# Kernel optimization log

Measured on AMD Instinct MI355X. Metric: run time of the kernel, lower is better.

The kernel has to match this reference:

```python
import jax, jax.numpy as jnp
import numpy as np

B, C, H, W = 4, 256, 64, 64

def setup_inputs() -> dict:
    key = jax.random.key(0)
    ks = jax.random.split(key, 6)
    inv = 1.0 / np.sqrt(C)
    return {
        "feature": jax.random.normal(ks[0], (B, C, H, W), dtype=jnp.float32),
        "flow": jax.random.normal(ks[1], (B, 2, H, W), dtype=jnp.float32),
        "q_w": jax.random.uniform(ks[2], (C, C), dtype=jnp.float32, minval=-inv, maxval=inv),
        "q_b": jax.random.uniform(ks[3], (C,), dtype=jnp.float32, minval=-inv, maxval=inv),
        "k_w": jax.random.uniform(ks[4], (C, C), dtype=jnp.float32, minval=-inv, maxval=inv),
        "k_b": jax.random.uniform(ks[5], (C,), dtype=jnp.float32, minval=-inv, maxval=inv),
    }

def reference(feature, flow, q_w, q_b, k_w, k_b):
    b, c, h, w = feature.shape
    # [b,c,h,w] -> [b, h*w, c] tokens
    tok = feature.reshape(b, c, h * w).transpose(0, 2, 1)
    v = flow.reshape(b, 2, h * w).transpose(0, 2, 1)       # [b, hw, 2]
    q = jnp.einsum('bnc,dc->bnd', tok, q_w) + q_b           # Linear(c,c)
    k = jnp.einsum('bnc,dc->bnd', tok, k_w) + k_b
    scale = 1.0 / jnp.sqrt(jnp.asarray(c, dtype=q.dtype))
    scores = jnp.einsum('bld,bsd->bls', q, k) * scale       # [b, hw, hw]
    attn = jax.nn.softmax(scores, axis=-1)                  # dropout_p=0 -> no-op
    out = jnp.einsum('bls,bsv->blv', attn, v)               # [b, hw, 2]
    return out.reshape(b, h, w, 2).transpose(0, 3, 1, 2)    # [b, 2, h, w]
```

## Files before the change

### kernel.cpp

```cpp
#include <hip/hip_runtime.h>
#include <math.h>

#define BB 4
#define CC 256
#define HWN 4096
#define NTOK 16384
#define SCQ 0.09016844136f

typedef __attribute__((ext_vector_type(8))) short short8;
typedef __attribute__((ext_vector_type(4))) float f32x4;
typedef unsigned short ushort_t;

__device__ __forceinline__ ushort_t f2bf(float f) {
    unsigned int u = __float_as_uint(f);
    unsigned int r = (u + 0x7FFFu + ((u >> 16) & 1u)) >> 16;
    return (ushort_t)r;
}
__device__ __forceinline__ unsigned int pack2(float a, float b) {
    return (unsigned int)f2bf(a) | ((unsigned int)f2bf(b) << 16);
}

__global__ __launch_bounds__(256, 2) void proj_kernel(
    const float* __restrict__ feature,
    const float* __restrict__ q_w, const float* __restrict__ k_w,
    const float* __restrict__ q_bias, const float* __restrict__ k_bias,
    ushort_t* __restrict__ qb, ushort_t* __restrict__ kb,
    float* __restrict__ zbuf)
{
    int gid = blockIdx.x * 256 + threadIdx.x;
    if (gid < 3 * NTOK) zbuf[gid] = 0.f;

    int tt = blockIdx.x & 63;
    int b  = blockIdx.x >> 6;
    int tok0 = tt * 64;

    int t = threadIdx.x, w = t >> 6, lane = t & 63;
    int n16 = lane & 15, quad = lane >> 4;

    __shared__ float    lsA[64][69];
    __shared__ ushort_t lsB[64][264];

    const float* F = feature + (size_t)(b * CC) * HWN;

    int cl = t >> 2, tg = (t & 3) * 16;
    int tokw = t >> 2, c16 = (t & 3) * 16;

    for (int ch = 0; ch < 4; ch++) {
        const float* src = F + (size_t)(ch * 64 + cl) * HWN + tok0 + tg;
        *(float4*)&lsA[cl][tg]      = *(const float4*)(src);
        *(float4*)&lsA[cl][tg + 4]  = *(const float4*)(src + 4);
        *(float4*)&lsA[cl][tg + 8]  = *(const float4*)(src + 8);
        *(float4*)&lsA[cl][tg + 12] = *(const float4*)(src + 12);
        __syncthreads();
        #pragma unroll
        for (int jj = 0; jj < 8; jj++)
            *(unsigned int*)&lsB[tokw][ch * 64 + c16 + 2 * jj] =
                pack2(lsA[c16 + 2 * jj][tokw], lsA[c16 + 2 * jj + 1][tokw]);
        __syncthreads();
    }

    int dw0 = w * 64;
    #pragma unroll
    for (int dsub = 0; dsub < 4; dsub++) {
        int d0 = dw0 + dsub * 16;
        f32x4 accq[4], acck[4];
        #pragma unroll
        for (int i = 0; i < 4; i++) {
            accq[i] = (f32x4){0.f, 0.f, 0.f, 0.f};
            acck[i] = (f32x4){0.f, 0.f, 0.f, 0.f};
        }
        #pragma unroll
        for (int kc = 0; kc < 8; kc++) {
            size_t off = (size_t)(d0 + n16) * CC + kc * 32 + quad * 8;
            float4 a0 = *(const float4*)&q_w[off];
            float4 a1 = *(const float4*)&q_w[off + 4];
            short8 aq, ak;
            aq[0] = (short)f2bf(a0.x * SCQ); aq[1] = (short)f2bf(a0.y * SCQ);
            aq[2] = (short)f2bf(a0.z * SCQ); aq[3] = (short)f2bf(a0.w * SCQ);
            aq[4] = (short)f2bf(a1.x * SCQ); aq[5] = (short)f2bf(a1.y * SCQ);
            aq[6] = (short)f2bf(a1.z * SCQ); aq[7] = (short)f2bf(a1.w * SCQ);
            a0 = *(const float4*)&k_w[off];
            a1 = *(const float4*)&k_w[off + 4];
            ak[0] = (short)f2bf(a0.x); ak[1] = (short)f2bf(a0.y);
            ak[2] = (short)f2bf(a0.z); ak[3] = (short)f2bf(a0.w);
            ak[4] = (short)f2bf(a1.x); ak[5] = (short)f2bf(a1.y);
            ak[6] = (short)f2bf(a1.z); ak[7] = (short)f2bf(a1.w);
            #pragma unroll
            for (int tokt = 0; tokt < 4; tokt++) {
                short8 bf = *(const short8*)&lsB[tokt * 16 + n16][kc * 32 + quad * 8];
                accq[tokt] = __builtin_amdgcn_mfma_f32_16x16x32_bf16(aq, bf, accq[tokt], 0, 0, 0);
                acck[tokt] = __builtin_amdgcn_mfma_f32_16x16x32_bf16(ak, bf, acck[tokt], 0, 0, 0);
            }
        }
        float bqv[4], bkv[4];
        #pragma unroll
        for (int r = 0; r < 4; r++) {
            bqv[r] = q_bias[d0 + quad * 4 + r] * SCQ;
            bkv[r] = k_bias[d0 + quad * 4 + r];
        }
        #pragma unroll
        for (int tokt = 0; tokt < 4; tokt++) {
            size_t row = (size_t)(b * HWN + tok0 + tokt * 16 + n16) * CC + d0 + quad * 4;
            ushort4 oq, ok;
            oq.x = f2bf(accq[tokt][0] + bqv[0]); oq.y = f2bf(accq[tokt][1] + bqv[1]);
            oq.z = f2bf(accq[tokt][2] + bqv[2]); oq.w = f2bf(accq[tokt][3] + bqv[3]);
            ok.x = f2bf(acck[tokt][0] + bkv[0]); ok.y = f2bf(acck[tokt][1] + bkv[1]);
            ok.z = f2bf(acck[tokt][2] + bkv[2]); ok.w = f2bf(acck[tokt][3] + bkv[3]);
            *(ushort4*)&qb[row] = oq;
            *(ushort4*)&kb[row] = ok;
        }
    }
}

__global__ __launch_bounds__(256, 2) void attn_kernel(
    const ushort_t* __restrict__ qb, const ushort_t* __restrict__ kb,
    const float* __restrict__ flow,
    float* __restrict__ den_g, float* __restrict__ nx_g, float* __restrict__ ny_g)
{
    int id = blockIdx.x;
    int qt = id & 15; id >>= 4;
    int sr = id & 7;  id >>= 3;
    int b = id;

    int t = threadIdx.x;
    int w = t >> 6, lane = t & 63;
    int n16 = lane & 15, quad = lane >> 4;

    int q0 = qt * 256 + w * 64;
    int s_beg = sr * 512;

    const ushort_t* Qb = qb + (size_t)b * HWN * CC;
    const ushort_t* Kb = kb + (size_t)b * HWN * CC;

    __shared__ __align__(16) ushort_t lk[2][8192];
    __shared__ float lflow[1024];

    const float* fx = flow + (size_t)b * 2 * HWN;
    const float* fy = fx + HWN;
    lflow[t]        = fx[s_beg + t];
    lflow[t + 256]  = fx[s_beg + t + 256];
    lflow[t + 512]  = fy[s_beg + t];
    lflow[t + 768]  = fy[s_beg + t + 256];

    short8 qf[4][8];
    #pragma unroll
    for (int tq = 0; tq < 4; tq++)
        #pragma unroll
        for (int c = 0; c < 8; c++)
            qf[tq][c] = *(const short8*)&Qb[(size_t)(q0 + tq * 16 + n16) * CC
                                            + c * 32 + quad * 8];

    int srcoff[4];
    #pragma unroll
    for (int i = 0; i < 4; i++) {
        int G = i * 256 + t;
        int r = G >> 5, j = G & 31;
        srcoff[i] = (r * 32 + (j ^ r)) * 16;
    }
    int p16[8];
    #pragma unroll
    for (int c = 0; c < 8; c++)
        p16[c] = (((c * 4 + quad) ^ n16) & 31) * 16;

    float den[4][4], nxa[4][4], nya[4][4];
    #pragma unroll
    for (int tq = 0; tq < 4; tq++)
        #pragma unroll
        for (int r = 0; r < 4; r++) { den[tq][r] = 0.f; nxa[tq][r] = 0.f; nya[tq][r] = 0.f; }

    {
        const char* gsrc = (const char*)(Kb + (size_t)s_beg * CC);
        char* ldst = (char*)lk[0] + t * 16;
        #pragma unroll
        for (int i = 0; i < 4; i++)
            __builtin_amdgcn_global_load_lds(
                (const __attribute__((address_space(1))) unsigned int*)(gsrc + srcoff[i]),
                (__attribute__((address_space(3))) unsigned int*)(ldst + i * 4096),
                16, 0, 0);
    }

    for (int st = 0; st < 16; st++) {
        __syncthreads();
        if (st + 1 < 16) {
            const char* gsrc = (const char*)(Kb + (size_t)(s_beg + (st + 1) * 32) * CC);
            char* ldst = (char*)lk[(st + 1) & 1] + t * 16;
            #pragma unroll
            for (int i = 0; i < 4; i++)
                __builtin_amdgcn_global_load_lds(
                    (const __attribute__((address_space(1))) unsigned int*)(gsrc + srcoff[i]),
                    (__attribute__((address_space(3))) unsigned int*)(ldst + i * 4096),
                    16, 0, 0);
        }
        const char* base = (const char*)lk[st & 1];

        #pragma unroll
        for (int bt = 0; bt < 2; bt++) {
            int rbase = (bt * 16 + n16) * 512;
            int x16   = bt ? 256 : 0;
            f32x4 a0 = {0.f, 0.f, 0.f, 0.f};
            f32x4 a1 = {0.f, 0.f, 0.f, 0.f};
            f32x4 a2 = {0.f, 0.f, 0.f, 0.f};
            f32x4 a3 = {0.f, 0.f, 0.f, 0.f};
            #pragma unroll
            for (int c = 0; c < 8; c++) {
                short8 kf = *(const short8*)(base + rbase + (p16[c] ^ x16));
                a0 = __builtin_amdgcn_mfma_f32_16x16x32_bf16(qf[0][c], kf, a0, 0, 0, 0);
                a1 = __builtin_amdgcn_mfma_f32_16x16x32_bf16(qf[1][c], kf, a1, 0, 0, 0);
                a2 = __builtin_amdgcn_mfma_f32_16x16x32_bf16(qf[2][c], kf, a2, 0, 0, 0);
                a3 = __builtin_amdgcn_mfma_f32_16x16x32_bf16(qf[3][c], kf, a3, 0, 0, 0);
            }
            int sidx = st * 32 + bt * 16 + n16;
            float vx = lflow[sidx];
            float vy = lflow[512 + sidx];
            #pragma unroll
            for (int r = 0; r < 4; r++) {
                float p0 = exp2f(a0[r]);
                float p1 = exp2f(a1[r]);
                float p2 = exp2f(a2[r]);
                float p3 = exp2f(a3[r]);
                den[0][r] += p0; den[1][r] += p1; den[2][r] += p2; den[3][r] += p3;
                nxa[0][r] = fmaf(p0, vx, nxa[0][r]); nxa[1][r] = fmaf(p1, vx, nxa[1][r]);
                nxa[2][r] = fmaf(p2, vx, nxa[2][r]); nxa[3][r] = fmaf(p3, vx, nxa[3][r]);
                nya[0][r] = fmaf(p0, vy, nya[0][r]); nya[1][r] = fmaf(p1, vy, nya[1][r]);
                nya[2][r] = fmaf(p2, vy, nya[2][r]); nya[3][r] = fmaf(p3, vy, nya[3][r]);
            }
        }
    }

    #pragma unroll
    for (int tq = 0; tq < 4; tq++)
        #pragma unroll
        for (int r = 0; r < 4; r++) {
            #pragma unroll
            for (int off = 8; off >= 1; off >>= 1) {
                den[tq][r] += __shfl_down(den[tq][r], off, 16);
                nxa[tq][r] += __shfl_down(nxa[tq][r], off, 16);
                nya[tq][r] += __shfl_down(nya[tq][r], off, 16);
            }
        }
    if (n16 == 0) {
        #pragma unroll
        for (int tq = 0; tq < 4; tq++)
            #pragma unroll
            for (int r = 0; r < 4; r++) {
                int qrow = q0 + tq * 16 + quad * 4 + r;
                int gi = b * HWN + qrow;
                atomicAdd(&den_g[gi], den[tq][r]);
                atomicAdd(&nx_g[gi],  nxa[tq][r]);
                atomicAdd(&ny_g[gi],  nya[tq][r]);
            }
    }
}

__global__ __launch_bounds__(256) void finalize_kernel(
    const float* __restrict__ den_g, const float* __restrict__ nx_g,
    const float* __restrict__ ny_g, float* __restrict__ out)
{
    int idx = blockIdx.x * 256 + threadIdx.x;
    int b = idx >> 12, n = idx & 4095;
    float inv = 1.0f / den_g[idx];
    out[(size_t)b * 2 * HWN + n]       = nx_g[idx] * inv;
    out[(size_t)b * 2 * HWN + HWN + n] = ny_g[idx] * inv;
}

extern "C" void kernel_launch(void* const* d_in, const int* in_sizes, int n_in,
                              void* d_out, int out_size, void* d_ws, size_t ws_size,
                              hipStream_t stream) {
    const float* feature = (const float*)d_in[0];
    const float* flow    = (const float*)d_in[1];
    const float* q_w     = (const float*)d_in[2];
    const float* q_b     = (const float*)d_in[3];
    const float* k_w     = (const float*)d_in[4];
    const float* k_b     = (const float*)d_in[5];
    float* out = (float*)d_out;

    ushort_t* qbuf = (ushort_t*)d_ws;
    ushort_t* kbuf = qbuf + (size_t)NTOK * CC;
    float* den = (float*)(kbuf + (size_t)NTOK * CC);
    float* nx  = den + NTOK;
    float* ny  = nx + NTOK;

    proj_kernel<<<256, 256, 0, stream>>>(feature, q_w, k_w, q_b, k_b,
                                         qbuf, kbuf, den);
    attn_kernel<<<512, 256, 0, stream>>>(qbuf, kbuf, flow, den, nx, ny);
    finalize_kernel<<<64, 256, 0, stream>>>(den, nx, ny, out);
}
```

Baseline: 141.2 us.

## Pre-convert weights, shrink projection tiles, drop LDS staging, fuse finalize into attention

Adds a kernel that converts the Q/K weights to bf16 once and zeroes the accumulators and counters, so the projection kernel no longer converts fp32 weights inside every block. The projection kernel now uses 32-token tiles across 512 blocks and prefetches the next weight fragments into registers. The attention kernel drops its LDS double-buffering and reads K and flow straight from global memory into registers. The finalize kernel is removed: a per-tile atomic counter lets the last split-block normalize and write the output. The trade-offs are more uncoalesced global K traffic and reliance on correct acquire/release ordering of the counter.

```diff
diff --git a/kernel.cpp b/kernel.cpp
--- a/kernel.cpp
+++ b/kernel.cpp
@@ -6,6 +6,7 @@
 #define HWN 4096
 #define NTOK 16384
 #define SCQ 0.09016844136f
+#define NZERO (3 * NTOK + 64)
 
 typedef __attribute__((ext_vector_type(8))) short short8;
 typedef __attribute__((ext_vector_type(4))) float f32x4;
@@ -20,76 +21,103 @@
     return (unsigned int)f2bf(a) | ((unsigned int)f2bf(b) << 16);
 }
 
+__global__ __launch_bounds__(256) void wconv_kernel(
+    const float* __restrict__ q_w, const float* __restrict__ k_w,
+    ushort_t* __restrict__ wq, ushort_t* __restrict__ wk,
+    float* __restrict__ zbuf)
+{
+    int bid = blockIdx.x, t = threadIdx.x;
+    if (bid < 32) {
+        int i = (bid * 256 + t) * 8;
+        float4 a = *(const float4*)&q_w[i];
+        float4 b = *(const float4*)&q_w[i + 4];
+        uint4 o;
+        o.x = pack2(a.x * SCQ, a.y * SCQ); o.y = pack2(a.z * SCQ, a.w * SCQ);
+        o.z = pack2(b.x * SCQ, b.y * SCQ); o.w = pack2(b.z * SCQ, b.w * SCQ);
+        *(uint4*)&wq[i] = o;
+        a = *(const float4*)&k_w[i];
+        b = *(const float4*)&k_w[i + 4];
+        o.x = pack2(a.x, a.y); o.y = pack2(a.z, a.w);
+        o.z = pack2(b.x, b.y); o.w = pack2(b.z, b.w);
+        *(uint4*)&wk[i] = o;
+    } else {
+        int base = (bid - 32) * 256 + t;
+        if (base < NZERO) zbuf[base] = 0.f;
+    }
+}
+
 __global__ __launch_bounds__(256, 2) void proj_kernel(
     const float* __restrict__ feature,
-    const float* __restrict__ q_w, const float* __restrict__ k_w,
+    const ushort_t* __restrict__ wq, const ushort_t* __restrict__ wk,
     const float* __restrict__ q_bias, const float* __restrict__ k_bias,
-    ushort_t* __restrict__ qb, ushort_t* __restrict__ kb,
-    float* __restrict__ zbuf)
+    ushort_t* __restrict__ qb, ushort_t* __restrict__ kb)
 {
-    int gid = blockIdx.x * 256 + threadIdx.x;
-    if (gid < 3 * NTOK) zbuf[gid] = 0.f;
-
-    int tt = blockIdx.x & 63;
-    int b  = blockIdx.x >> 6;
-    int tok0 = tt * 64;
+    int tt = blockIdx.x & 127;
+    int b  = blockIdx.x >> 7;
+    int tok0 = tt * 32;
 
     int t = threadIdx.x, w = t >> 6, lane = t & 63;
     int n16 = lane & 15, quad = lane >> 4;
 
-    __shared__ float    lsA[64][69];
-    __shared__ ushort_t lsB[64][264];
+    __shared__ float    lsA[64][34];
+    __shared__ ushort_t lsB[32][264];
 
     const float* F = feature + (size_t)(b * CC) * HWN;
 
-    int cl = t >> 2, tg = (t & 3) * 16;
-    int tokw = t >> 2, c16 = (t & 3) * 16;
+    int cl = t >> 2, tg = (t & 3) * 8;
+    int tokw = t >> 3, c8 = (t & 7) * 8;
 
     for (int ch = 0; ch < 4; ch++) {
         const float* src = F + (size_t)(ch * 64 + cl) * HWN + tok0 + tg;
-        *(float4*)&lsA[cl][tg]      = *(const float4*)(src);
-        *(float4*)&lsA[cl][tg + 4]  = *(const float4*)(src + 4);
-        *(float4*)&lsA[cl][tg + 8]  = *(const float4*)(src + 8);
-        *(float4*)&lsA[cl][tg + 12] = *(const float4*)(src + 12);
+        float4 v0 = *(const float4*)src;
+        float4 v1 = *(const float4*)(src + 4);
+        *(float2*)&lsA[cl][tg]     = make_float2(v0.x, v0.y);
+        *(float2*)&lsA[cl][tg + 2] = make_float2(v0.z, v0.w);
+        *(float2*)&lsA[cl][tg + 4] = make_float2(v1.x, v1.y);
+        *(float2*)&lsA[cl][tg + 6] = make_float2(v1.z, v1.w);
         __syncthreads();
-        #pragma unroll
-        for (int jj = 0; jj < 8; jj++)
-            *(unsigned int*)&lsB[tokw][ch * 64 + c16 + 2 * jj] =
-                pack2(lsA[c16 + 2 * jj][tokw], lsA[c16 + 2 * jj + 1][tokw]);
+        uint4 o;
+        o.x = pack2(lsA[c8 + 0][tokw], lsA[c8 + 1][tokw]);
+        o.y = pack2(lsA[c8 + 2][tokw], lsA[c8 + 3][tokw]);
+        o.z = pack2(lsA[c8 + 4][tokw], lsA[c8 + 5][tokw]);
+        o.w = pack2(lsA[c8 + 6][tokw], lsA[c8 + 7][tokw]);
+        *(uint4*)&lsB[tokw][ch * 64 + c8] = o;
         __syncthreads();
     }
 
     int dw0 = w * 64;
+    short8 aq[8], ak[8], aq2[8], ak2[8];
+    #pragma unroll
+    for (int kc = 0; kc < 8; kc++) {
+        size_t off = (size_t)(dw0 + n16) * CC + kc * 32 + quad * 8;
+        aq[kc] = *(const short8*)&wq[off];
+        ak[kc] = *(const short8*)&wk[off];
+    }
+
     #pragma unroll
     for (int dsub = 0; dsub < 4; dsub++) {
         int d0 = dw0 + dsub * 16;
-        f32x4 accq[4], acck[4];
-        #pragma unroll
-        for (int i = 0; i < 4; i++) {
+        if (dsub < 3) {
+            #pragma unroll
+            for (int kc = 0; kc < 8; kc++) {
+                size_t off = (size_t)(d0 + 16 + n16) * CC + kc * 32 + quad * 8;
+                aq2[kc] = *(const short8*)&wq[off];
+                ak2[kc] = *(const short8*)&wk[off];
+            }
+        }
+        f32x4 accq[2], acck[2];
+        #pragma unroll
+        for (int i = 0; i < 2; i++) {
             accq[i] = (f32x4){0.f, 0.f, 0.f, 0.f};
             acck[i] = (f32x4){0.f, 0.f, 0.f, 0.f};
         }
         #pragma unroll
         for (int kc = 0; kc < 8; kc++) {
-            size_t off = (size_t)(d0 + n16) * CC + kc * 32 + quad * 8;
-            float4 a0 = *(const float4*)&q_w[off];
-            float4 a1 = *(const float4*)&q_w[off + 4];
-            short8 aq, ak;
-            aq[0] = (short)f2bf(a0.x * SCQ); aq[1] = (short)f2bf(a0.y * SCQ);
-            aq[2] = (short)f2bf(a0.z * SCQ); aq[3] = (short)f2bf(a0.w * SCQ);
-            aq[4] = (short)f2bf(a1.x * SCQ); aq[5] = (short)f2bf(a1.y * SCQ);
-            aq[6] = (short)f2bf(a1.z * SCQ); aq[7] = (short)f2bf(a1.w * SCQ);
-            a0 = *(const float4*)&k_w[off];
-            a1 = *(const float4*)&k_w[off + 4];
-            ak[0] = (short)f2bf(a0.x); ak[1] = (short)f2bf(a0.y);
-            ak[2] = (short)f2bf(a0.z); ak[3] = (short)f2bf(a0.w);
-            ak[4] = (short)f2bf(a1.x); ak[5] = (short)f2bf(a1.y);
-            ak[6] = (short)f2bf(a1.z); ak[7] = (short)f2bf(a1.w);
-            #pragma unroll
-            for (int tokt = 0; tokt < 4; tokt++) {
+            #pragma unroll
+            for (int tokt = 0; tokt < 2; tokt++) {
                 short8 bf = *(const short8*)&lsB[tokt * 16 + n16][kc * 32 + quad * 8];
-                accq[tokt] = __builtin_amdgcn_mfma_f32_16x16x32_bf16(aq, bf, accq[tokt], 0, 0, 0);
-                acck[tokt] = __builtin_amdgcn_mfma_f32_16x16x32_bf16(ak, bf, acck[tokt], 0, 0, 0);
+                accq[tokt] = __builtin_amdgcn_mfma_f32_16x16x32_bf16(aq[kc], bf, accq[tokt], 0, 0, 0);
+                acck[tokt] = __builtin_amdgcn_mfma_f32_16x16x32_bf16(ak[kc], bf, acck[tokt], 0, 0, 0);
             }
         }
         float bqv[4], bkv[4];
@@ -99,7 +127,7 @@
             bkv[r] = k_bias[d0 + quad * 4 + r];
         }
         #pragma unroll
-        for (int tokt = 0; tokt < 4; tokt++) {
+        for (int tokt = 0; tokt < 2; tokt++) {
             size_t row = (size_t)(b * HWN + tok0 + tokt * 16 + n16) * CC + d0 + quad * 4;
             ushort4 oq, ok;
             oq.x = f2bf(accq[tokt][0] + bqv[0]); oq.y = f2bf(accq[tokt][1] + bqv[1]);
@@ -109,13 +137,16 @@
             *(ushort4*)&qb[row] = oq;
             *(ushort4*)&kb[row] = ok;
         }
+        #pragma unroll
+        for (int kc = 0; kc < 8; kc++) { aq[kc] = aq2[kc]; ak[kc] = ak2[kc]; }
     }
 }
 
 __global__ __launch_bounds__(256, 2) void attn_kernel(
     const ushort_t* __restrict__ qb, const ushort_t* __restrict__ kb,
     const float* __restrict__ flow,
-    float* __restrict__ den_g, float* __restrict__ nx_g, float* __restrict__ ny_g)
+    float* __restrict__ den_g, float* __restrict__ nx_g, float* __restrict__ ny_g,
+    int* __restrict__ cnt_g, float* __restrict__ out)
 {
     int id = blockIdx.x;
     int qt = id & 15; id >>= 4;
@@ -131,16 +162,8 @@
 
     const ushort_t* Qb = qb + (size_t)b * HWN * CC;
     const ushort_t* Kb = kb + (size_t)b * HWN * CC;
-
-    __shared__ __align__(16) ushort_t lk[2][8192];
-    __shared__ float lflow[1024];
-
     const float* fx = flow + (size_t)b * 2 * HWN;
     const float* fy = fx + HWN;
-    lflow[t]        = fx[s_beg + t];
-    lflow[t + 256]  = fx[s_beg + t + 256];
-    lflow[t + 512]  = fy[s_beg + t];
-    lflow[t + 768]  = fy[s_beg + t + 256];
 
     short8 qf[4][8];
     #pragma unroll
@@ -150,80 +173,43 @@
             qf[tq][c] = *(const short8*)&Qb[(size_t)(q0 + tq * 16 + n16) * CC
                                             + c * 32 + quad * 8];
 
-    int srcoff[4];
-    #pragma unroll
-    for (int i = 0; i < 4; i++) {
-        int G = i * 256 + t;
-        int r = G >> 5, j = G & 31;
-        srcoff[i] = (r * 32 + (j ^ r)) * 16;
-    }
-    int p16[8];
-    #pragma unroll
-    for (int c = 0; c < 8; c++)
-        p16[c] = (((c * 4 + quad) ^ n16) & 31) * 16;
-
     float den[4][4], nxa[4][4], nya[4][4];
     #pragma unroll
     for (int tq = 0; tq < 4; tq++)
         #pragma unroll
         for (int r = 0; r < 4; r++) { den[tq][r] = 0.f; nxa[tq][r] = 0.f; nya[tq][r] = 0.f; }
 
-    {
-        const char* gsrc = (const char*)(Kb + (size_t)s_beg * CC);
-        char* ldst = (char*)lk[0] + t * 16;
-        #pragma unroll
-        for (int i = 0; i < 4; i++)
-            __builtin_amdgcn_global_load_lds(
-                (const __attribute__((address_space(1))) unsigned int*)(gsrc + srcoff[i]),
-                (__attribute__((address_space(3))) unsigned int*)(ldst + i * 4096),
-                16, 0, 0);
-    }
-
-    for (int st = 0; st < 16; st++) {
-        __syncthreads();
-        if (st + 1 < 16) {
-            const char* gsrc = (const char*)(Kb + (size_t)(s_beg + (st + 1) * 32) * CC);
-            char* ldst = (char*)lk[(st + 1) & 1] + t * 16;
-            #pragma unroll
-            for (int i = 0; i < 4; i++)
-                __builtin_amdgcn_global_load_lds(
-                    (const __attribute__((address_space(1))) unsigned int*)(gsrc + srcoff[i]),
-                    (__attribute__((address_space(3))) unsigned int*)(ldst + i * 4096),
-                    16, 0, 0);
-        }
-        const char* base = (const char*)lk[st & 1];
-
-        #pragma unroll
-        for (int bt = 0; bt < 2; bt++) {
-            int rbase = (bt * 16 + n16) * 512;
-            int x16   = bt ? 256 : 0;
-            f32x4 a0 = {0.f, 0.f, 0.f, 0.f};
-            f32x4 a1 = {0.f, 0.f, 0.f, 0.f};
-            f32x4 a2 = {0.f, 0.f, 0.f, 0.f};
-            f32x4 a3 = {0.f, 0.f, 0.f, 0.f};
-            #pragma unroll
-            for (int c = 0; c < 8; c++) {
-                short8 kf = *(const short8*)(base + rbase + (p16[c] ^ x16));
-                a0 = __builtin_amdgcn_mfma_f32_16x16x32_bf16(qf[0][c], kf, a0, 0, 0, 0);
-                a1 = __builtin_amdgcn_mfma_f32_16x16x32_bf16(qf[1][c], kf, a1, 0, 0, 0);
-                a2 = __builtin_amdgcn_mfma_f32_16x16x32_bf16(qf[2][c], kf, a2, 0, 0, 0);
-                a3 = __builtin_amdgcn_mfma_f32_16x16x32_bf16(qf[3][c], kf, a3, 0, 0, 0);
-            }
-            int sidx = st * 32 + bt * 16 + n16;
-            float vx = lflow[sidx];
-            float vy = lflow[512 + sidx];
-            #pragma unroll
-            for (int r = 0; r < 4; r++) {
-                float p0 = exp2f(a0[r]);
-                float p1 = exp2f(a1[r]);
-                float p2 = exp2f(a2[r]);
-                float p3 = exp2f(a3[r]);
-                den[0][r] += p0; den[1][r] += p1; den[2][r] += p2; den[3][r] += p3;
-                nxa[0][r] = fmaf(p0, vx, nxa[0][r]); nxa[1][r] = fmaf(p1, vx, nxa[1][r]);
-                nxa[2][r] = fmaf(p2, vx, nxa[2][r]); nxa[3][r] = fmaf(p3, vx, nxa[3][r]);
-                nya[0][r] = fmaf(p0, vy, nya[0][r]); nya[1][r] = fmaf(p1, vy, nya[1][r]);
-                nya[2][r] = fmaf(p2, vy, nya[2][r]); nya[3][r] = fmaf(p3, vy, nya[3][r]);
-            }
+    for (int st = 0; st < 32; st++) {
+        int s0 = s_beg + st * 16;
+        short8 kf[8];
+        #pragma unroll
+        for (int c = 0; c < 8; c++)
+            kf[c] = *(const short8*)&Kb[(size_t)(s0 + n16) * CC + c * 32 + quad * 8];
+        float vx = fx[s0 + n16];
+        float vy = fy[s0 + n16];
+
+        f32x4 a0 = {0.f, 0.f, 0.f, 0.f};
+        f32x4 a1 = {0.f, 0.f, 0.f, 0.f};
+        f32x4 a2 = {0.f, 0.f, 0.f, 0.f};
+        f32x4 a3 = {0.f, 0.f, 0.f, 0.f};
+        #pragma unroll
+        for (int c = 0; c < 8; c++) {
+            a0 = __builtin_amdgcn_mfma_f32_16x16x32_bf16(qf[0][c], kf[c], a0, 0, 0, 0);
+            a1 = __builtin_amdgcn_mfma_f32_16x16x32_bf16(qf[1][c], kf[c], a1, 0, 0, 0);
+            a2 = __builtin_amdgcn_mfma_f32_16x16x32_bf16(qf[2][c], kf[c], a2, 0, 0, 0);
+            a3 = __builtin_amdgcn_mfma_f32_16x16x32_bf16(qf[3][c], kf[c], a3, 0, 0, 0);
+        }
+        #pragma unroll
+        for (int r = 0; r < 4; r++) {
+            float p0 = exp2f(a0[r]);
+            float p1 = exp2f(a1[r]);
+            float p2 = exp2f(a2[r]);
+            float p3 = exp2f(a3[r]);
+            den[0][r] += p0; den[1][r] += p1; den[2][r] += p2; den[3][r] += p3;
+            nxa[0][r] = fmaf(p0, vx, nxa[0][r]); nxa[1][r] = fmaf(p1, vx, nxa[1][r]);
+            nxa[2][r] = fmaf(p2, vx, nxa[2][r]); nxa[3][r] = fmaf(p3, vx, nxa[3][r]);
+            nya[0][r] = fmaf(p0, vy, nya[0][r]); nya[1][r] = fmaf(p1, vy, nya[1][r]);
+            nya[2][r] = fmaf(p2, vy, nya[2][r]); nya[3][r] = fmaf(p3, vy, nya[3][r]);
         }
     }
 
@@ -250,17 +236,27 @@
                 atomicAdd(&ny_g[gi],  nya[tq][r]);
             }
     }
-}
-
-__global__ __launch_bounds__(256) void finalize_kernel(
-    const float* __restrict__ den_g, const float* __restrict__ nx_g,
-    const float* __restrict__ ny_g, float* __restrict__ out)
-{
-    int idx = blockIdx.x * 256 + threadIdx.x;
-    int b = idx >> 12, n = idx & 4095;
-    float inv = 1.0f / den_g[idx];
-    out[(size_t)b * 2 * HWN + n]       = nx_g[idx] * inv;
-    out[(size_t)b * 2 * HWN + HWN + n] = ny_g[idx] * inv;
+
+    __shared__ int is_last;
+    __syncthreads();
+    if (t == 0) {
+        __threadfence();
+        int old = __hip_atomic_fetch_add(&cnt_g[b * 16 + qt], 1,
+                                         __ATOMIC_ACQ_REL, __HIP_MEMORY_SCOPE_AGENT);
+        is_last = (old == 7);
+    }
+    __syncthreads();
+    if (is_last) {
+        __threadfence();
+        int qrow = qt * 256 + t;
+        int gi = b * HWN + qrow;
+        float d = __hip_atomic_load(&den_g[gi], __ATOMIC_RELAXED, __HIP_MEMORY_SCOPE_AGENT);
+        float x = __hip_atomic_load(&nx_g[gi],  __ATOMIC_RELAXED, __HIP_MEMORY_SCOPE_AGENT);
+        float y = __hip_atomic_load(&ny_g[gi],  __ATOMIC_RELAXED, __HIP_MEMORY_SCOPE_AGENT);
+        float inv = 1.0f / d;
+        out[(size_t)b * 2 * HWN + qrow]       = x * inv;
+        out[(size_t)b * 2 * HWN + HWN + qrow] = y * inv;
+    }
 }
 
 extern "C" void kernel_launch(void* const* d_in, const int* in_sizes, int n_in,
@@ -276,12 +272,14 @@
 
     ushort_t* qbuf = (ushort_t*)d_ws;
     ushort_t* kbuf = qbuf + (size_t)NTOK * CC;
-    float* den = (float*)(kbuf + (size_t)NTOK * CC);
+    ushort_t* wq   = kbuf + (size_t)NTOK * CC;
+    ushort_t* wk   = wq + (size_t)CC * CC;
+    float* den = (float*)(wk + (size_t)CC * CC);
     float* nx  = den + NTOK;
     float* ny  = nx + NTOK;
-
-    proj_kernel<<<256, 256, 0, stream>>>(feature, q_w, k_w, q_b, k_b,
-                                         qbuf, kbuf, den);
-    attn_kernel<<<512, 256, 0, stream>>>(qbuf, kbuf, flow, den, nx, ny);
-    finalize_kernel<<<64, 256, 0, stream>>>(den, nx, ny, out);
-}
+    int*   cnt = (int*)(ny + NTOK);
+
+    wconv_kernel<<<256, 256, 0, stream>>>(q_w, k_w, wq, wk, den);
+    proj_kernel<<<512, 256, 0, stream>>>(feature, wq, wk, q_b, k_b, qbuf, kbuf);
+    attn_kernel<<<512, 256, 0, stream>>>(qbuf, kbuf, flow, den, nx, ny, cnt, out);
+}
```

Result: slower. 183.7 us (+30.1%).
